# Performance work log

Hardware: AMD Instinct MI355X
Metric: run time of the kernel (lower is better)

Reference implementation:

```python
import jax, jax.numpy as jnp
import numpy as np

B = 1048576
STATE_D, ACT_D = 12, 6
IN_D = STATE_D + ACT_D  # 18
W_HID = 10
N_HID = 19  # num_layers - 1 hidden->hidden layers
OUT_D = 1
SLOPE = 0.1


def setup_inputs() -> dict:
    key = jax.random.key(0)
    ks = jax.random.split(key, 8)
    s = 0.1
    return {
        "state": jax.random.normal(ks[0], (B, STATE_D), dtype=jnp.float32),
        "action": jax.random.normal(ks[1], (B, ACT_D), dtype=jnp.float32),
        "W0": jax.random.normal(ks[2], (W_HID, IN_D), dtype=jnp.float32) * s,
        "b0": jax.random.normal(ks[3], (W_HID,), dtype=jnp.float32) * s,
        "Ws": jax.random.normal(ks[4], (N_HID, W_HID, W_HID), dtype=jnp.float32) * s,
        "bs": jax.random.normal(ks[5], (N_HID, W_HID), dtype=jnp.float32) * s,
        "Wf": jax.random.normal(ks[6], (OUT_D, W_HID), dtype=jnp.float32) * s,
        "bf": jax.random.normal(ks[7], (OUT_D,), dtype=jnp.float32) * s,
    }


def _lrelu(x):
    return jnp.where(x >= 0, x, SLOPE * x)


def reference(state, action, W0, b0, Ws, bs, Wf, bf):
    x = jnp.concatenate((state, action), axis=1)  # [B, 18]
    h = _lrelu(x @ W0.T + b0)                     # [B, 10]

    def layer(h, wb):
        W, b = wb
        return _lrelu(h @ W.T + b), None

    h, _ = jax.lax.scan(layer, h, (Ws, bs))       # 19 hidden layers
    out = _lrelu(h @ Wf.T + bf)                   # [B, 1]
    return out.T                                  # [1, B]
```

## Files before the change

### kernel.cpp

```cpp
#include <hip/hip_runtime.h>

typedef float v2f __attribute__((ext_vector_type(2)));

constexpr int IN_D = 18, W_HID = 10, N_HID = 19;
constexpr float SLOPE = 0.1f;

__device__ __forceinline__ v2f splat(float s) { v2f v; v[0] = s; v[1] = s; return v; }

__device__ __forceinline__ v2f lrelu2(v2f x) {
    return __builtin_elementwise_max(x, x * splat(SLOPE));
}

__device__ __forceinline__ void layer10(const v2f* __restrict__ in, v2f* __restrict__ outv,
                                        const float* __restrict__ W, const float* __restrict__ bb) {
    #pragma unroll
    for (int j = 0; j < W_HID; ++j) {
        v2f acc = splat(bb[j]);
        #pragma unroll
        for (int k = 0; k < W_HID; ++k)
            acc = __builtin_elementwise_fma(in[k], splat(W[j*W_HID + k]), acc);
        outv[j] = lrelu2(acc);
    }
}

__global__ __launch_bounds__(256, 4) void critic_pk2r4(
    const float* __restrict__ state, const float* __restrict__ action,
    const float* __restrict__ W0, const float* __restrict__ bias0,
    const float* __restrict__ Ws, const float* __restrict__ bs,
    const float* __restrict__ Wf, const float* __restrict__ bf,
    float* __restrict__ out, int B)
{
    const int t = blockIdx.x * blockDim.x + threadIdx.x;
    if (t * 2 >= B) return;

    float Sf[24];
    {
        const float4* s4 = reinterpret_cast<const float4*>(state) + (size_t)t * 6;
        #pragma unroll
        for (int r = 0; r < 6; ++r) {
            float4 v = s4[r];
            Sf[4*r] = v.x; Sf[4*r+1] = v.y; Sf[4*r+2] = v.z; Sf[4*r+3] = v.w;
        }
    }
    float Af[12];
    {
        const float4* a4 = reinterpret_cast<const float4*>(action) + (size_t)t * 3;
        #pragma unroll
        for (int r = 0; r < 3; ++r) {
            float4 v = a4[r];
            Af[4*r] = v.x; Af[4*r+1] = v.y; Af[4*r+2] = v.z; Af[4*r+3] = v.w;
        }
    }

    v2f x[IN_D];
    #pragma unroll
    for (int k = 0; k < 12; ++k) { v2f v; v[0] = Sf[k]; v[1] = Sf[12 + k]; x[k] = v; }
    #pragma unroll
    for (int k = 0; k < 6; ++k)  { v2f v; v[0] = Af[k]; v[1] = Af[6 + k];  x[12 + k] = v; }

    v2f h[W_HID], g[W_HID];
    #pragma unroll
    for (int j = 0; j < W_HID; ++j) {
        v2f acc = splat(bias0[j]);
        #pragma unroll
        for (int k = 0; k < IN_D; ++k)
            acc = __builtin_elementwise_fma(x[k], splat(W0[j*IN_D + k]), acc);
        h[j] = lrelu2(acc);
    }

    const float* __restrict__ W  = Ws;
    const float* __restrict__ bb = bs;
    #pragma unroll 1
    for (int it = 0; it < (N_HID - 1) / 2; ++it) {
        layer10(h, g, W,               bb);
        layer10(g, h, W + W_HID*W_HID, bb + W_HID);
        W  += 2 * W_HID * W_HID;
        bb += 2 * W_HID;
    }
    layer10(h, g, W, bb);

    v2f acc = splat(bf[0]);
    #pragma unroll
    for (int k = 0; k < W_HID; ++k)
        acc = __builtin_elementwise_fma(g[k], splat(Wf[k]), acc);
    acc = lrelu2(acc);

    float2 o; o.x = acc[0]; o.y = acc[1];
    reinterpret_cast<float2*>(out)[t] = o;
}

extern "C" void kernel_launch(void* const* d_in, const int* in_sizes, int n_in,
                              void* d_out, int out_size, void* d_ws, size_t ws_size,
                              hipStream_t stream) {
    const float* state  = (const float*)d_in[0];
    const float* action = (const float*)d_in[1];
    const float* W0     = (const float*)d_in[2];
    const float* b0     = (const float*)d_in[3];
    const float* Ws     = (const float*)d_in[4];
    const float* bs     = (const float*)d_in[5];
    const float* Wf     = (const float*)d_in[6];
    const float* bf     = (const float*)d_in[7];
    float* out = (float*)d_out;

    const int B = out_size;
    const int nthreads = B / 2;
    const int block = 256;
    const int grid = (nthreads + block - 1) / block;
    critic_pk2r4<<<grid, block, 0, stream>>>(state, action, W0, b0, Ws, bs, Wf, bf, out, B);
}
```

Measured before the change: 59.12 us.

## Process eight rows per thread to amortize scalar weight loads

```diff
diff --git a/kernel.cpp b/kernel.cpp
--- a/kernel.cpp
+++ b/kernel.cpp
@@ -11,31 +11,41 @@
     return __builtin_elementwise_max(x, x * splat(SLOPE));
 }
 
-__device__ __forceinline__ void layer10(const v2f* __restrict__ in, v2f* __restrict__ outv,
-                                        const float* __restrict__ W, const float* __restrict__ bb) {
+__device__ __forceinline__ void layer10_x4(
+    const v2f* __restrict__ iA, v2f* __restrict__ oA,
+    const v2f* __restrict__ iB, v2f* __restrict__ oB,
+    const v2f* __restrict__ iC, v2f* __restrict__ oC,
+    const v2f* __restrict__ iD, v2f* __restrict__ oD,
+    const float* __restrict__ W, const float* __restrict__ bb)
+{
     #pragma unroll
     for (int j = 0; j < W_HID; ++j) {
-        v2f acc = splat(bb[j]);
+        v2f aA = splat(bb[j]);
+        v2f aB = aA, aC = aA, aD = aA;
         #pragma unroll
-        for (int k = 0; k < W_HID; ++k)
-            acc = __builtin_elementwise_fma(in[k], splat(W[j*W_HID + k]), acc);
-        outv[j] = lrelu2(acc);
+        for (int k = 0; k < W_HID; ++k) {
+            const float w = W[j*W_HID + k];
+            v2f wv = splat(w);
+            aA = __builtin_elementwise_fma(iA[k], wv, aA);
+            aB = __builtin_elementwise_fma(iB[k], wv, aB);
+            aC = __builtin_elementwise_fma(iC[k], wv, aC);
+            aD = __builtin_elementwise_fma(iD[k], wv, aD);
+        }
+        oA[j] = lrelu2(aA);
+        oB[j] = lrelu2(aB);
+        oC[j] = lrelu2(aC);
+        oD[j] = lrelu2(aD);
     }
 }
 
-__global__ __launch_bounds__(256, 4) void critic_pk2r4(
+__device__ __forceinline__ void load_and_layer0(
     const float* __restrict__ state, const float* __restrict__ action,
     const float* __restrict__ W0, const float* __restrict__ bias0,
-    const float* __restrict__ Ws, const float* __restrict__ bs,
-    const float* __restrict__ Wf, const float* __restrict__ bf,
-    float* __restrict__ out, int B)
+    int pairIdx, v2f* __restrict__ h)
 {
-    const int t = blockIdx.x * blockDim.x + threadIdx.x;
-    if (t * 2 >= B) return;
-
     float Sf[24];
     {
-        const float4* s4 = reinterpret_cast<const float4*>(state) + (size_t)t * 6;
+        const float4* s4 = reinterpret_cast<const float4*>(state) + (size_t)pairIdx * 6;
         #pragma unroll
         for (int r = 0; r < 6; ++r) {
             float4 v = s4[r];
@@ -44,21 +54,19 @@
     }
     float Af[12];
     {
-        const float4* a4 = reinterpret_cast<const float4*>(action) + (size_t)t * 3;
+        const float4* a4 = reinterpret_cast<const float4*>(action) + (size_t)pairIdx * 3;
         #pragma unroll
         for (int r = 0; r < 3; ++r) {
             float4 v = a4[r];
             Af[4*r] = v.x; Af[4*r+1] = v.y; Af[4*r+2] = v.z; Af[4*r+3] = v.w;
         }
     }
-
     v2f x[IN_D];
     #pragma unroll
     for (int k = 0; k < 12; ++k) { v2f v; v[0] = Sf[k]; v[1] = Sf[12 + k]; x[k] = v; }
     #pragma unroll
     for (int k = 0; k < 6; ++k)  { v2f v; v[0] = Af[k]; v[1] = Af[6 + k];  x[12 + k] = v; }
 
-    v2f h[W_HID], g[W_HID];
     #pragma unroll
     for (int j = 0; j < W_HID; ++j) {
         v2f acc = splat(bias0[j]);
@@ -67,26 +75,55 @@
             acc = __builtin_elementwise_fma(x[k], splat(W0[j*IN_D + k]), acc);
         h[j] = lrelu2(acc);
     }
+}
+
+__global__ __launch_bounds__(256, 2) void critic_pk8(
+    const float* __restrict__ state, const float* __restrict__ action,
+    const float* __restrict__ W0, const float* __restrict__ bias0,
+    const float* __restrict__ Ws, const float* __restrict__ bs,
+    const float* __restrict__ Wf, const float* __restrict__ bf,
+    float* __restrict__ out, int B)
+{
+    const int t = blockIdx.x * blockDim.x + threadIdx.x;
+    if (t * 8 >= B) return;
+    const int pair0 = t * 4;
+
+    v2f hA[W_HID], hB[W_HID], hC[W_HID], hD[W_HID];
+    v2f gA[W_HID], gB[W_HID], gC[W_HID], gD[W_HID];
+
+    load_and_layer0(state, action, W0, bias0, pair0 + 0, hA);
+    load_and_layer0(state, action, W0, bias0, pair0 + 1, hB);
+    load_and_layer0(state, action, W0, bias0, pair0 + 2, hC);
+    load_and_layer0(state, action, W0, bias0, pair0 + 3, hD);
 
     const float* __restrict__ W  = Ws;
     const float* __restrict__ bb = bs;
     #pragma unroll 1
     for (int it = 0; it < (N_HID - 1) / 2; ++it) {
-        layer10(h, g, W,               bb);
-        layer10(g, h, W + W_HID*W_HID, bb + W_HID);
+        layer10_x4(hA, gA, hB, gB, hC, gC, hD, gD, W,               bb);
+        layer10_x4(gA, hA, gB, hB, gC, hC, gD, hD, W + W_HID*W_HID, bb + W_HID);
         W  += 2 * W_HID * W_HID;
         bb += 2 * W_HID;
     }
-    layer10(h, g, W, bb);
+    layer10_x4(hA, gA, hB, gB, hC, gC, hD, gD, W, bb);
 
-    v2f acc = splat(bf[0]);
+    v2f aA = splat(bf[0]);
+    v2f aB = aA, aC = aA, aD = aA;
     #pragma unroll
-    for (int k = 0; k < W_HID; ++k)
-        acc = __builtin_elementwise_fma(g[k], splat(Wf[k]), acc);
-    acc = lrelu2(acc);
+    for (int k = 0; k < W_HID; ++k) {
+        v2f wv = splat(Wf[k]);
+        aA = __builtin_elementwise_fma(gA[k], wv, aA);
+        aB = __builtin_elementwise_fma(gB[k], wv, aB);
+        aC = __builtin_elementwise_fma(gC[k], wv, aC);
+        aD = __builtin_elementwise_fma(gD[k], wv, aD);
+    }
+    aA = lrelu2(aA); aB = lrelu2(aB); aC = lrelu2(aC); aD = lrelu2(aD);
 
-    float2 o; o.x = acc[0]; o.y = acc[1];
-    reinterpret_cast<float2*>(out)[t] = o;
+    float4 o0; o0.x = aA[0]; o0.y = aA[1]; o0.z = aB[0]; o0.w = aB[1];
+    float4 o1; o1.x = aC[0]; o1.y = aC[1]; o1.z = aD[0]; o1.w = aD[1];
+    float4* op = reinterpret_cast<float4*>(out) + (size_t)t * 2;
+    op[0] = o0;
+    op[1] = o1;
 }
 
 extern "C" void kernel_launch(void* const* d_in, const int* in_sizes, int n_in,
@@ -103,8 +140,8 @@
     float* out = (float*)d_out;
 
     const int B = out_size;
-    const int nthreads = B / 2;
+    const int nthreads = B / 8;
     const int block = 256;
     const int grid = (nthreads + block - 1) / block;
-    critic_pk2r4<<<grid, block, 0, stream>>>(state, action, W0, b0, Ws, bs, Wf, bf, out, B);
+    critic_pk8<<<grid, block, 0, stream>>>(state, action, W0, b0, Ws, bs, Wf, bf, out, B);
 }
```

Result: slower. 66.23 us (+12.0%).

## Stage duplicated weight pairs in LDS and use inline packed FMA

Applied to the files above, without the earlier changes.

```diff
diff --git a/kernel.cpp b/kernel.cpp
--- a/kernel.cpp
+++ b/kernel.cpp
@@ -1,37 +1,79 @@
 #include <hip/hip_runtime.h>
 
 typedef float v2f __attribute__((ext_vector_type(2)));
+typedef float v4f __attribute__((ext_vector_type(4)));
 
 constexpr int IN_D = 18, W_HID = 10, N_HID = 19;
 constexpr float SLOPE = 0.1f;
 
-__device__ __forceinline__ v2f splat(float s) { v2f v; v[0] = s; v[1] = s; return v; }
+constexpr int P_H = 0, P_L0 = 2280, P_F = 2480, N_PAIRS = 2492;
 
-__device__ __forceinline__ v2f lrelu2(v2f x) {
-    return __builtin_elementwise_max(x, x * splat(SLOPE));
+__device__ __forceinline__ v2f pk_fma(v2f acc, v2f x, v2f w) {
+    asm("v_pk_fma_f32 %0, %1, %2, %0" : "+v"(acc) : "v"(x), "v"(w));
+    return acc;
 }
+__device__ __forceinline__ v2f pk_lrelu(v2f x, v2f slope2) {
+    v2f y;
+    asm("v_pk_mul_f32 %0, %1, %2" : "=v"(y) : "v"(x), "v"(slope2));
+    v2f r;
+    r[0] = fmaxf(x[0], y[0]);
+    r[1] = fmaxf(x[1], y[1]);
+    return r;
+}
+#define SHUF(q, a, b) __builtin_shufflevector((q), (q), (a), (b))
 
-__device__ __forceinline__ void layer10(const v2f* __restrict__ in, v2f* __restrict__ outv,
-                                        const float* __restrict__ W, const float* __restrict__ bb) {
+__device__ __forceinline__ void layer10_lds(const v2f* __restrict__ in, v2f* __restrict__ outv,
+                                            const float2* __restrict__ lrow, v2f slope2) {
     #pragma unroll
     for (int j = 0; j < W_HID; ++j) {
-        v2f acc = splat(bb[j]);
-        #pragma unroll
-        for (int k = 0; k < W_HID; ++k)
-            acc = __builtin_elementwise_fma(in[k], splat(W[j*W_HID + k]), acc);
-        outv[j] = lrelu2(acc);
+        const v4f* rp = reinterpret_cast<const v4f*>(lrow + j * 12);
+        v4f q0 = rp[0], q1 = rp[1], q2 = rp[2], q3 = rp[3], q4 = rp[4], q5 = rp[5];
+        v2f acc = SHUF(q5, 0, 1);
+        acc = pk_fma(acc, in[0], SHUF(q0, 0, 1));
+        acc = pk_fma(acc, in[1], SHUF(q0, 2, 3));
+        acc = pk_fma(acc, in[2], SHUF(q1, 0, 1));
+        acc = pk_fma(acc, in[3], SHUF(q1, 2, 3));
+        acc = pk_fma(acc, in[4], SHUF(q2, 0, 1));
+        acc = pk_fma(acc, in[5], SHUF(q2, 2, 3));
+        acc = pk_fma(acc, in[6], SHUF(q3, 0, 1));
+        acc = pk_fma(acc, in[7], SHUF(q3, 2, 3));
+        acc = pk_fma(acc, in[8], SHUF(q4, 0, 1));
+        acc = pk_fma(acc, in[9], SHUF(q4, 2, 3));
+        outv[j] = pk_lrelu(acc, slope2);
     }
 }
 
-__global__ __launch_bounds__(256, 4) void critic_pk2r4(
+__global__ __launch_bounds__(256, 4) void critic_pk_ldsdup(
     const float* __restrict__ state, const float* __restrict__ action,
-    const float* __restrict__ W0, const float* __restrict__ bias0,
+    const float* __restrict__ W0, const float* __restrict__ b0,
     const float* __restrict__ Ws, const float* __restrict__ bs,
     const float* __restrict__ Wf, const float* __restrict__ bf,
     float* __restrict__ out, int B)
 {
-    const int t = blockIdx.x * blockDim.x + threadIdx.x;
+    __shared__ float2 lw[N_PAIRS];
+    const int tid = threadIdx.x;
+
+    for (int idx = tid; idx < 1900; idx += 256) {
+        int l = idx / 100, rem = idx % 100, r = rem / 10, c = rem % 10;
+        float w = Ws[idx]; lw[P_H + l * 120 + r * 12 + c] = make_float2(w, w);
+    }
+    for (int idx = tid; idx < 190; idx += 256) {
+        int l = idx / 10, r = idx % 10;
+        float w = bs[idx]; lw[P_H + l * 120 + r * 12 + 10] = make_float2(w, w);
+    }
+    for (int idx = tid; idx < 180; idx += 256) {
+        int r = idx / 18, c = idx % 18;
+        float w = W0[idx]; lw[P_L0 + r * 20 + c] = make_float2(w, w);
+    }
+    if (tid < 10)  { float w = b0[tid]; lw[P_L0 + tid * 20 + 18] = make_float2(w, w); }
+    if (tid >= 32 && tid < 42) { float w = Wf[tid - 32]; lw[P_F + (tid - 32)] = make_float2(w, w); }
+    if (tid == 64) { float w = bf[0]; lw[P_F + 10] = make_float2(w, w); }
+    __syncthreads();
+
+    const int t = blockIdx.x * blockDim.x + tid;
     if (t * 2 >= B) return;
+
+    const v2f slope2 = {SLOPE, SLOPE};
 
     float Sf[24];
     {
@@ -51,7 +93,6 @@
             Af[4*r] = v.x; Af[4*r+1] = v.y; Af[4*r+2] = v.z; Af[4*r+3] = v.w;
         }
     }
-
     v2f x[IN_D];
     #pragma unroll
     for (int k = 0; k < 12; ++k) { v2f v; v[0] = Sf[k]; v[1] = Sf[12 + k]; x[k] = v; }
@@ -61,32 +102,58 @@
     v2f h[W_HID], g[W_HID];
     #pragma unroll
     for (int j = 0; j < W_HID; ++j) {
-        v2f acc = splat(bias0[j]);
-        #pragma unroll
-        for (int k = 0; k < IN_D; ++k)
-            acc = __builtin_elementwise_fma(x[k], splat(W0[j*IN_D + k]), acc);
-        h[j] = lrelu2(acc);
+        const v4f* rp = reinterpret_cast<const v4f*>(lw + P_L0 + j * 20);
+        v4f q0 = rp[0], q1 = rp[1], q2 = rp[2], q3 = rp[3], q4 = rp[4];
+        v4f q5 = rp[5], q6 = rp[6], q7 = rp[7], q8 = rp[8], q9 = rp[9];
+        v2f acc = SHUF(q9, 0, 1);
+        acc = pk_fma(acc, x[0],  SHUF(q0, 0, 1));
+        acc = pk_fma(acc, x[1],  SHUF(q0, 2, 3));
+        acc = pk_fma(acc, x[2],  SHUF(q1, 0, 1));
+        acc = pk_fma(acc, x[3],  SHUF(q1, 2, 3));
+        acc = pk_fma(acc, x[4],  SHUF(q2, 0, 1));
+        acc = pk_fma(acc, x[5],  SHUF(q2, 2, 3));
+        acc = pk_fma(acc, x[6],  SHUF(q3, 0, 1));
+        acc = pk_fma(acc, x[7],  SHUF(q3, 2, 3));
+        acc = pk_fma(acc, x[8],  SHUF(q4, 0, 1));
+        acc = pk_fma(acc, x[9],  SHUF(q4, 2, 3));
+        acc = pk_fma(acc, x[10], SHUF(q5, 0, 1));
+        acc = pk_fma(acc, x[11], SHUF(q5, 2, 3));
+        acc = pk_fma(acc, x[12], SHUF(q6, 0, 1));
+        acc = pk_fma(acc, x[13], SHUF(q6, 2, 3));
+        acc = pk_fma(acc, x[14], SHUF(q7, 0, 1));
+        acc = pk_fma(acc, x[15], SHUF(q7, 2, 3));
+        acc = pk_fma(acc, x[16], SHUF(q8, 0, 1));
+        acc = pk_fma(acc, x[17], SHUF(q8, 2, 3));
+        h[j] = pk_lrelu(acc, slope2);
     }
 
-    const float* __restrict__ W  = Ws;
-    const float* __restrict__ bb = bs;
+    const float2* lb = lw + P_H;
     #pragma unroll 1
     for (int it = 0; it < (N_HID - 1) / 2; ++it) {
-        layer10(h, g, W,               bb);
-        layer10(g, h, W + W_HID*W_HID, bb + W_HID);
-        W  += 2 * W_HID * W_HID;
-        bb += 2 * W_HID;
+        layer10_lds(h, g, lb,       slope2);
+        layer10_lds(g, h, lb + 120, slope2);
+        lb += 240;
     }
-    layer10(h, g, W, bb);
+    layer10_lds(h, g, lb, slope2);
 
-    v2f acc = splat(bf[0]);
-    #pragma unroll
-    for (int k = 0; k < W_HID; ++k)
-        acc = __builtin_elementwise_fma(g[k], splat(Wf[k]), acc);
-    acc = lrelu2(acc);
-
-    float2 o; o.x = acc[0]; o.y = acc[1];
-    reinterpret_cast<float2*>(out)[t] = o;
+    {
+        const v4f* rp = reinterpret_cast<const v4f*>(lw + P_F);
+        v4f q0 = rp[0], q1 = rp[1], q2 = rp[2], q3 = rp[3], q4 = rp[4], q5 = rp[5];
+        v2f acc = SHUF(q5, 0, 1);
+        acc = pk_fma(acc, g[0], SHUF(q0, 0, 1));
+        acc = pk_fma(acc, g[1], SHUF(q0, 2, 3));
+        acc = pk_fma(acc, g[2], SHUF(q1, 0, 1));
+        acc = pk_fma(acc, g[3], SHUF(q1, 2, 3));
+        acc = pk_fma(acc, g[4], SHUF(q2, 0, 1));
+        acc = pk_fma(acc, g[5], SHUF(q2, 2, 3));
+        acc = pk_fma(acc, g[6], SHUF(q3, 0, 1));
+        acc = pk_fma(acc, g[7], SHUF(q3, 2, 3));
+        acc = pk_fma(acc, g[8], SHUF(q4, 0, 1));
+        acc = pk_fma(acc, g[9], SHUF(q4, 2, 3));
+        acc = pk_lrelu(acc, slope2);
+        float2 o; o.x = acc[0]; o.y = acc[1];
+        reinterpret_cast<float2*>(out)[t] = o;
+    }
 }
 
 extern "C" void kernel_launch(void* const* d_in, const int* in_sizes, int n_in,
@@ -106,5 +173,5 @@
     const int nthreads = B / 2;
     const int block = 256;
     const int grid = (nthreads + block - 1) / block;
-    critic_pk2r4<<<grid, block, 0, stream>>>(state, action, W0, b0, Ws, bs, Wf, bf, out, B);
+    critic_pk_ldsdup<<<grid, block, 0, stream>>>(state, action, W0, b0, Ws, bs, Wf, bf, out, B);
 }
```

Measured after the change: 88.43 us. 49.6% more time.
